# Kernel tuning notes

Hardware: AMD Instinct MI355X
Metric: run time of the kernel (lower is better)

The kernel has to match this reference:

```python
import jax, jax.numpy as jnp
import numpy as np
import math

B, H, W = 4, 128, 128
D_MODEL, D_HEAD, N_HEADS = 256, 64, 4
COND, D_FF = 256, 512
WS, SHIFT = 8, 4
EPS = 1e-6


def _make_masks(n_h, n_w, wh, ww, shift):
    # Swin-style shifted-window attention mask, vectorized (matches make_shifted_window_masks)
    ph = np.arange(n_h)[:, None, None, None, None, None]
    pw = np.arange(n_w)[None, :, None, None, None, None]
    qh = np.arange(wh)[None, None, :, None, None, None]
    qw = np.arange(ww)[None, None, None, :, None, None]
    kh = np.arange(wh)[None, None, None, None, :, None]
    kw = np.arange(ww)[None, None, None, None, None, :]
    is_top, is_left = ph == 0, pw == 0
    qa, ka, ql, kl = qh < shift, kh < shift, qw < shift, kw < shift
    m = ((is_left & is_top & (ql == kl) & (qa == ka))
         | (is_left & ~is_top & (ql == kl))
         | (~is_left & is_top & (qa == ka))
         | (~is_left & ~is_top))
    m = np.broadcast_to(m, (n_h, n_w, wh, ww, wh, ww))
    return jnp.asarray(m.reshape(n_h, n_w, wh * ww, wh * ww))


def _rms_norm(x, scale):
    ms = jnp.mean(jnp.square(x), -1, keepdims=True)
    return x * (scale * jax.lax.rsqrt(ms + EPS))


def _rope(x, theta):
    # rotate first 2*d dims of x (d = theta.shape[-1]), pass rest through
    d = theta.shape[-1]
    x1, x2, rest = x[..., :d], x[..., d:2 * d], x[..., 2 * d:]
    c, s = jnp.cos(theta), jnp.sin(theta)
    return jnp.concatenate([x1 * c - x2 * s, x2 * c + x1 * s, rest], axis=-1)


def setup_inputs() -> dict:
    key = jax.random.key(0)
    ks = jax.random.split(key, 10)
    x = jax.random.normal(ks[0], (B, H, W, D_MODEL), jnp.float32)
    gh = jnp.linspace(-1.0, 1.0, H)
    gw = jnp.linspace(-1.0, 1.0, W)
    pos = jnp.stack(jnp.meshgrid(gh, gw, indexing='ij'), axis=-1)  # [H,W,2]
    pos = jnp.broadcast_to(pos, (B, H, W, 2)).astype(jnp.float32)
    cond = jax.random.normal(ks[1], (B, COND), jnp.float32)
    # AdaRMSNorm linears are zero-init in torch; use small random so scale ~ 1
    norm1_w = 0.02 * jax.random.normal(ks[2], (D_MODEL, COND), jnp.float32)
    norm2_w = 0.02 * jax.random.normal(ks[3], (D_MODEL, COND), jnp.float32)
    qkv_w = jax.random.normal(ks[4], (3 * D_MODEL, D_MODEL), jnp.float32) / math.sqrt(D_MODEL)
    out_w = jax.random.normal(ks[5], (D_MODEL, D_MODEL), jnp.float32) / math.sqrt(D_MODEL)
    up_w = jax.random.normal(ks[6], (2 * D_FF, D_MODEL), jnp.float32) / math.sqrt(D_MODEL)
    down_w = jax.random.normal(ks[7], (D_MODEL, D_FF), jnp.float32) / math.sqrt(D_FF)
    scale_attn = jnp.full((N_HEADS,), 10.0, jnp.float32)
    # AxialRoPE freqs buffer: dim = d_head // 2
    dim = D_HEAD // 2
    f = np.exp(np.linspace(math.log(math.pi), math.log(10.0 * math.pi), N_HEADS * dim // 4 + 1)[:-1])
    freqs = jnp.asarray(f.reshape(dim // 4, N_HEADS).T, dtype=jnp.float32)  # [n_heads, d_head//8]
    return {"x": x, "pos": pos, "cond": cond, "norm1_w": norm1_w, "qkv_w": qkv_w,
            "scale_attn": scale_attn, "freqs": freqs, "out_w": out_w,
            "norm2_w": norm2_w, "up_w": up_w, "down_w": down_w}


def reference(x, pos, cond, norm1_w, qkv_w, scale_attn, freqs, out_w, norm2_w, up_w, down_w):
    b, h, w, dm = x.shape
    # --- shifted-window self-attention block ---
    skip = x
    xn = _rms_norm(x, (cond @ norm1_w.T + 1.0)[:, None, None, :])
    qkv = (xn @ qkv_w.T).reshape(b, h, w, 3, N_HEADS, D_HEAD)
    qkv = jnp.transpose(qkv, (3, 0, 4, 1, 2, 5))  # [3, b, nh, h, w, dh]
    q, k, v = qkv[0], qkv[1], qkv[2]
    # cosine-sim QK scaling with learned per-head scale
    s = jnp.sqrt(scale_attn)[None, :, None, None, None]
    q = q * (s * jax.lax.rsqrt(jnp.sum(q * q, -1, keepdims=True) + EPS))
    k = k * (s * jax.lax.rsqrt(jnp.sum(k * k, -1, keepdims=True) + EPS))
    # axial RoPE
    theta_h = pos[..., None, 0:1] * freqs  # [b,h,w,nh,dh//8]
    theta_w = pos[..., None, 1:2] * freqs
    theta = jnp.moveaxis(jnp.concatenate([theta_h, theta_w], -1), -2, -4)  # [b,nh,h,w,dh//4]
    q = _rope(q, theta)
    k = _rope(k, theta)
    # shifted windowing: roll, then partition into WS x WS windows
    def win(t):
        t = jnp.roll(t, (SHIFT, SHIFT), axis=(-3, -2))
        t = t.reshape(b, N_HEADS, h // WS, WS, w // WS, WS, D_HEAD)
        t = jnp.swapaxes(t, -4, -3)  # [b,nh,h',w',WS,WS,dh]
        return t.reshape(b, N_HEADS, h // WS, w // WS, WS * WS, D_HEAD)
    qw_, kw_, vw_ = win(q), win(k), win(v)
    mask = _make_masks(h // WS, w // WS, WS, WS, SHIFT)  # [h',w',S,S]
    scores = jnp.einsum('bnhwqd,bnhwkd->bnhwqk', qw_, kw_)  # sdpa scale=1.0 (cosine sim)
    scores = jnp.where(mask, scores, -1e30)
    attn = jax.nn.softmax(scores, axis=-1)
    o = jnp.einsum('bnhwqk,bnhwkd->bnhwqd', attn, vw_)
    # un-window and roll back
    o = o.reshape(b, N_HEADS, h // WS, w // WS, WS, WS, D_HEAD)
    o = jnp.swapaxes(o, -4, -3).reshape(b, N_HEADS, h, w, D_HEAD)
    o = jnp.roll(o, (-SHIFT, -SHIFT), axis=(-3, -2))
    o = jnp.transpose(o, (0, 2, 3, 1, 4)).reshape(b, h, w, dm)
    x = skip + o @ out_w.T
    # --- GEGLU feed-forward block ---
    skip = x
    xn = _rms_norm(x, (cond @ norm2_w.T + 1.0)[:, None, None, :])
    u = xn @ up_w.T
    a, g = u[..., :D_FF], u[..., D_FF:]
    x = skip + (a * jax.nn.gelu(g, approximate=False)) @ down_w.T
    return x
```

## Files before the change

kernel.cpp:

```cpp
#include <hip/hip_runtime.h>
#include <hip/hip_bf16.h>


using short8 = __attribute__((ext_vector_type(8))) short;
using f32x4  = __attribute__((ext_vector_type(4))) float;

#define DEVINL __device__ __forceinline__

DEVINL float bf2f(unsigned short u) {
    union { unsigned u; float f; } v; v.u = ((unsigned)u) << 16; return v.f;
}
DEVINL unsigned short f2bf(float f) {
    union { float f; unsigned u; } v; v.f = f;
    unsigned u = v.u;
    return (unsigned short)((u + 0x7FFFu + ((u >> 16) & 1u)) >> 16);
}
DEVINL void unpack8(uint4 pk, float* f) {
    unsigned w[4] = { pk.x, pk.y, pk.z, pk.w };
#pragma unroll
    for (int t = 0; t < 4; ++t) {
        union { unsigned u; float f; } lo, hi;
        lo.u = w[t] << 16; hi.u = w[t] & 0xffff0000u;
        f[2 * t] = lo.f; f[2 * t + 1] = hi.f;
    }
}
DEVINL void gload_lds16(const void* g, void* l) {
    __builtin_amdgcn_global_load_lds(
        (__attribute__((address_space(1))) void*)(unsigned long long)(uintptr_t)g,
        (__attribute__((address_space(3))) void*)(unsigned)(uintptr_t)l,
        16, 0, 0);
}

__global__ __launch_bounds__(256)
void wconv_kernel(const float* __restrict__ qkvw, const float* __restrict__ outw,
                  const float* __restrict__ upw, const float* __restrict__ downw,
                  unsigned short* __restrict__ dst)
{
    const int i = blockIdx.x * 256 + threadIdx.x;
    float v;
    if (i < 196608)      v = qkvw[i];
    else if (i < 262144) v = outw[i - 196608];
    else if (i < 524288) v = upw[i - 262144];
    else                 v = downw[i - 524288];
    dst[i] = f2bf(v);
}

__global__ __launch_bounds__(256)
void scales_kernel(const float* __restrict__ cond, const float* __restrict__ n1w,
                   const float* __restrict__ n2w, float* __restrict__ s1, float* __restrict__ s2)
{
    const int b = blockIdx.x & 3, which = blockIdx.x >> 2;
    const int c = threadIdx.x;
    const float* wrow = (which ? n2w : n1w) + (size_t)c * 256;
    const float* cb = cond + (size_t)b * 256;
    float acc = 0.f;
    for (int j = 0; j < 256; ++j) acc += cb[j] * wrow[j];
    (which ? s2 : s1)[b * 256 + c] = acc + 1.0f;
}

__global__ __launch_bounds__(256)
void rmsnorm_kernel(const float* __restrict__ x, const float* __restrict__ s,
                    unsigned short* __restrict__ out)
{
    const int t = blockIdx.x * 4 + (threadIdx.x >> 6);
    const int lane = threadIdx.x & 63;
    const float4 xv = *(const float4*)(x + (size_t)t * 256 + lane * 4);
    float ss = xv.x * xv.x + xv.y * xv.y + xv.z * xv.z + xv.w * xv.w;
#pragma unroll
    for (int off = 32; off; off >>= 1) ss += __shfl_xor(ss, off);
    const float rstd = rsqrtf(ss * (1.f / 256.f) + 1e-6f);
    const int b = t >> 14;
    const float4 sv = *(const float4*)(s + b * 256 + lane * 4);
    unsigned short o[4] = { f2bf(xv.x * sv.x * rstd), f2bf(xv.y * sv.y * rstd),
                            f2bf(xv.z * sv.z * rstd), f2bf(xv.w * sv.w * rstd) };
    *(uint2*)(out + (size_t)t * 256 + lane * 4) = *(uint2*)o;
}

template<int EPI>
__global__ __launch_bounds__(256)
void gemm_bt(const unsigned short* __restrict__ A, const unsigned short* __restrict__ Bw,
             const float* __restrict__ resid, void* __restrict__ outp,
             int M, int N, int K)
{
    __shared__ char smem[(EPI == 2) ? 49152 : 32768];
    const int tid = threadIdx.x;
    const int wave = tid >> 6, lane = tid & 63;
    const int n0 = blockIdx.x * 128;
    const int m0 = blockIdx.y * 128;
    const int wm = wave >> 1, wn = wave & 1;

    f32x4 acc[4][4] = {};
    f32x4 accg[4][4] = {};

    const int lrow8 = lane >> 3;
    const int skel = (lane & 7) * 8;

    for (int k0 = 0; k0 < K; k0 += 64) {
        __syncthreads();
#pragma unroll
        for (int i = 0; i < 4; ++i) {
            const int chunk = wave * 4 + i;
            const int row = chunk * 8 + lrow8;
            const unsigned short* ga = A  + (size_t)(m0 + row) * K + k0 + skel;
            const unsigned short* gb = Bw + (size_t)(n0 + row) * K + k0 + skel;
            gload_lds16(ga, smem + chunk * 1024);
            gload_lds16(gb, smem + 16384 + chunk * 1024);
            if constexpr (EPI == 2) {
                const unsigned short* gg = Bw + (size_t)(512 + n0 + row) * K + k0 + skel;
                gload_lds16(gg, smem + 32768 + chunk * 1024);
            }
        }
        __syncthreads();
#pragma unroll
        for (int kk = 0; kk < 2; ++kk) {
            const int kb = kk * 64 + (lane >> 4) * 16;
            short8 a[4], b[4], bg[4];
#pragma unroll
            for (int m = 0; m < 4; ++m)
                a[m] = *(const short8*)(smem + (wm * 64 + m * 16 + (lane & 15)) * 128 + kb);
#pragma unroll
            for (int n = 0; n < 4; ++n) {
                b[n] = *(const short8*)(smem + 16384 + (wn * 64 + n * 16 + (lane & 15)) * 128 + kb);
                if constexpr (EPI == 2)
                    bg[n] = *(const short8*)(smem + 32768 + (wn * 64 + n * 16 + (lane & 15)) * 128 + kb);
            }
#pragma unroll
            for (int m = 0; m < 4; ++m)
#pragma unroll
                for (int n = 0; n < 4; ++n) {
                    acc[m][n] = __builtin_amdgcn_mfma_f32_16x16x32_bf16(a[m], b[n], acc[m][n], 0, 0, 0);
                    if constexpr (EPI == 2)
                        accg[m][n] = __builtin_amdgcn_mfma_f32_16x16x32_bf16(a[m], bg[n], accg[m][n], 0, 0, 0);
                }
        }
    }
    const int rb = m0 + wm * 64 + ((lane >> 4) << 2);
    const int cb = n0 + wn * 64 + (lane & 15);
#pragma unroll
    for (int m = 0; m < 4; ++m)
#pragma unroll
        for (int n = 0; n < 4; ++n)
#pragma unroll
            for (int j = 0; j < 4; ++j) {
                const int row = rb + m * 16 + j;
                const int col = cb + n * 16;
                const size_t idx = (size_t)row * N + col;
                if constexpr (EPI == 0)
                    ((unsigned short*)outp)[idx] = f2bf(acc[m][n][j]);
                if constexpr (EPI == 1)
                    ((float*)outp)[idx] = resid[idx] + acc[m][n][j];
                if constexpr (EPI == 2) {
                    const float g = accg[m][n][j];
                    const float h = acc[m][n][j] * (0.5f * g * (1.0f + erff(g * 0.70710678118654752f)));
                    ((unsigned short*)outp)[idx] = f2bf(h);
                }
            }
}

__global__ __launch_bounds__(256)
void windowrope_kernel(const unsigned short* __restrict__ qkv, const float* __restrict__ pos,
                       const float* __restrict__ freqs, const float* __restrict__ sattn,
                       unsigned short* __restrict__ qw, unsigned short* __restrict__ kw,
                       unsigned short* __restrict__ vw)
{
    const int gid = blockIdx.x * 4 + (threadIdx.x >> 6);
    const int lane = threadIdx.x & 63;
    const int t = gid >> 2, n = gid & 3;
    const int b = t >> 14;
    const int h = (t >> 7) & 127, w = t & 127;

    const size_t base = (size_t)t * 768 + n * 64 + lane;
    float q = bf2f(qkv[base]);
    float k = bf2f(qkv[base + 256]);
    const float v = bf2f(qkv[base + 512]);

    float sq = q * q, sk = k * k;
#pragma unroll
    for (int off = 32; off; off >>= 1) { sq += __shfl_xor(sq, off); sk += __shfl_xor(sk, off); }
    const float sc = sqrtf(sattn[n]);
    q *= sc * rsqrtf(sq + 1e-6f);
    k *= sc * rsqrtf(sk + 1e-6f);

    const float qo = __shfl_xor(q, 16);
    const float ko = __shfl_xor(k, 16);
    if (lane < 32) {
        const int i = lane & 15;
        const float p = pos[(size_t)t * 2 + (i >> 3)];
        const float th = p * freqs[n * 8 + (i & 7)];
        float sth, cth;
        sincosf(th, &sth, &cth);
        if (lane < 16) { q = q * cth - qo * sth; k = k * cth - ko * sth; }
        else           { q = q * cth + qo * sth; k = k * cth + ko * sth; }
    }

    const int hr = (h + 4) & 127, wr = (w + 4) & 127;
    const int wh = hr >> 3, ww = wr >> 3;
    const int qp = (hr & 7) * 8 + (wr & 7);
    const size_t wbase = ((size_t)((b * 4 + n) * 256 + wh * 16 + ww) * 64 + qp) * 64 + lane;
    qw[wbase] = f2bf(q);
    kw[wbase] = f2bf(k);
    vw[wbase] = f2bf(v);
}

__global__ __launch_bounds__(64, 1)
void attn_kernel(const unsigned short* __restrict__ qw, const unsigned short* __restrict__ kw,
                 const unsigned short* __restrict__ vw, unsigned short* __restrict__ otok)
{
    __shared__ unsigned short Ks[4096];
    __shared__ unsigned short Vs[4096];
    const int bid = blockIdx.x;
    const int lane = threadIdx.x;
    const size_t wbase = (size_t)bid * 4096;

#pragma unroll
    for (int i = 0; i < 8; ++i) {
        const int idx = (i * 64 + lane) * 8;
        *(uint4*)(Ks + idx) = *(const uint4*)(kw + wbase + idx);
        *(uint4*)(Vs + idx) = *(const uint4*)(vw + wbase + idx);
    }
    float q[64];
#pragma unroll
    for (int i = 0; i < 8; ++i) {
        const uint4 pk = *(const uint4*)(qw + wbase + (size_t)lane * 64 + i * 8);
        unpack8(pk, q + i * 8);
    }
    __syncthreads();

    const int wh = (bid >> 4) & 15, ww = bid & 15;
    unsigned long long mask = ~0ull;
    if (wh == 0) mask &= (lane < 32) ? 0x00000000FFFFFFFFull : 0xFFFFFFFF00000000ull;
    if (ww == 0) mask &= ((lane & 7) < 4) ? 0x0F0F0F0F0F0F0F0Full : 0xF0F0F0F0F0F0F0F0ull;

    float o[64];
#pragma unroll
    for (int d = 0; d < 64; ++d) o[d] = 0.f;
    float sum = 0.f;

    for (int j = 0; j < 64; ++j) {
        float part[8];
#pragma unroll
        for (int dv = 0; dv < 8; ++dv) {
            const uint4 pk = *(const uint4*)(Ks + j * 64 + dv * 8);
            float f[8]; unpack8(pk, f);
            float a = 0.f;
#pragma unroll
            for (int u = 0; u < 8; ++u) a = fmaf(q[dv * 8 + u], f[u], a);
            part[dv] = a;
        }
        float s = ((part[0] + part[1]) + (part[2] + part[3])) +
                  ((part[4] + part[5]) + (part[6] + part[7]));
        float p = ((mask >> j) & 1ull) ? __expf(s - 10.f) : 0.f;
        sum += p;
#pragma unroll
        for (int dv = 0; dv < 8; ++dv) {
            const uint4 pk = *(const uint4*)(Vs + j * 64 + dv * 8);
            float f[8]; unpack8(pk, f);
#pragma unroll
            for (int u = 0; u < 8; ++u) o[dv * 8 + u] = fmaf(p, f[u], o[dv * 8 + u]);
        }
    }
    const float inv = 1.f / sum;

    const int b = bid >> 10, n = (bid >> 8) & 3;
    const int h = (wh * 8 + (lane >> 3) - 4) & 127;
    const int w = (ww * 8 + (lane & 7) - 4) & 127;
    unsigned short* dst = otok + ((size_t)(b * 128 + h) * 128 + w) * 256 + n * 64;
#pragma unroll
    for (int i = 0; i < 8; ++i) {
        unsigned short tmp[8];
#pragma unroll
        for (int u = 0; u < 8; ++u) tmp[u] = f2bf(o[i * 8 + u] * inv);
        *(uint4*)(dst + i * 8) = *(uint4*)tmp;
    }
}

extern "C" void kernel_launch(void* const* d_in, const int* in_sizes, int n_in,
                              void* d_out, int out_size, void* d_ws, size_t ws_size,
                              hipStream_t stream)
{
    (void)in_sizes; (void)n_in; (void)out_size; (void)ws_size;
    const float* x     = (const float*)d_in[0];
    const float* pos   = (const float*)d_in[1];
    const float* cond  = (const float*)d_in[2];
    const float* n1w   = (const float*)d_in[3];
    const float* qkvw  = (const float*)d_in[4];
    const float* sattn = (const float*)d_in[5];
    const float* freqs = (const float*)d_in[6];
    const float* outw  = (const float*)d_in[7];
    const float* n2w   = (const float*)d_in[8];
    const float* upw   = (const float*)d_in[9];
    const float* downw = (const float*)d_in[10];

    char* ws = (char*)d_ws;
    unsigned short* WB    = (unsigned short*)(ws);
    unsigned short* Wqkv  = WB;
    unsigned short* Wout  = WB + 196608;
    unsigned short* Wup   = WB + 262144;
    unsigned short* Wdown = WB + 524288;
    float* S1 = (float*)(ws + 1310720);
    float* S2 = (float*)(ws + 1314816);
    unsigned short* XN   = (unsigned short*)(ws + 2097152);
    unsigned short* QW   = (unsigned short*)(ws + 2097152);
    unsigned short* KW   = (unsigned short*)(ws + 35651584);
    unsigned short* VW   = (unsigned short*)(ws + 69206016);
    unsigned short* QKV  = (unsigned short*)(ws + 102760448);
    unsigned short* OTOK = (unsigned short*)(ws + 102760448);
    float*          X1   = (float*)(ws + 136314880);
    unsigned short* XN2  = (unsigned short*)(ws + 2097152);
    unsigned short* HG   = (unsigned short*)(ws + 35651584);

    wconv_kernel<<<2560, 256, 0, stream>>>(qkvw, outw, upw, downw, WB);
    scales_kernel<<<8, 256, 0, stream>>>(cond, n1w, n2w, S1, S2);
    rmsnorm_kernel<<<16384, 256, 0, stream>>>(x, S1, XN);
    gemm_bt<0><<<dim3(6, 512), 256, 0, stream>>>(XN, Wqkv, nullptr, QKV, 65536, 768, 256);
    windowrope_kernel<<<65536, 256, 0, stream>>>(QKV, pos, freqs, sattn, QW, KW, VW);
    attn_kernel<<<4096, 64, 0, stream>>>(QW, KW, VW, OTOK);
    gemm_bt<1><<<dim3(2, 512), 256, 0, stream>>>(OTOK, Wout, x, X1, 65536, 256, 256);
    rmsnorm_kernel<<<16384, 256, 0, stream>>>(X1, S2, XN2);
    gemm_bt<2><<<dim3(4, 512), 256, 0, stream>>>(XN2, Wup, nullptr, HG, 65536, 512, 256);
    gemm_bt<1><<<dim3(2, 512), 256, 0, stream>>>(HG, Wdown, X1, (float*)d_out, 65536, 256, 512);
}
```

Measured before the change: 623.2 us.

## Shrink GEMM N-tile to 64, add XOR-swizzled LDS, split up/gate GEMM

Halves the GEMM block tile in N from 128 to 64 and adds launch_bounds occupancy hints, which cuts accumulator registers and LDS per block so more blocks fit per CU. LDS rows are stored with an XOR swizzle, applied both on the global-to-LDS load and on the fragment reads, to avoid bank conflicts. The GEGLU up/gate GEMM moves into its own kernel with a 64-wide tile. The cost is twice as many blocks, each re-reading the A tile, so A-matrix global traffic doubles in exchange for better occupancy.

```diff
diff --git a/kernel.cpp b/kernel.cpp
--- a/kernel.cpp
+++ b/kernel.cpp
@@ -30,6 +30,7 @@
         (__attribute__((address_space(3))) void*)(unsigned)(uintptr_t)l,
         16, 0, 0);
 }
+DEVINL int swz(int row, int kb) { return row * 128 + (kb ^ ((row & 7) << 4)); }
 
 __global__ __launch_bounds__(256)
 void wconv_kernel(const float* __restrict__ qkvw, const float* __restrict__ outw,
@@ -77,69 +78,57 @@
 }
 
 template<int EPI>
-__global__ __launch_bounds__(256)
+__global__ __launch_bounds__(256, 4)
 void gemm_bt(const unsigned short* __restrict__ A, const unsigned short* __restrict__ Bw,
              const float* __restrict__ resid, void* __restrict__ outp,
              int M, int N, int K)
 {
-    __shared__ char smem[(EPI == 2) ? 49152 : 32768];
+    __shared__ char smem[24576];
     const int tid = threadIdx.x;
     const int wave = tid >> 6, lane = tid & 63;
-    const int n0 = blockIdx.x * 128;
+    const int n0 = blockIdx.x * 64;
     const int m0 = blockIdx.y * 128;
     const int wm = wave >> 1, wn = wave & 1;
 
-    f32x4 acc[4][4] = {};
-    f32x4 accg[4][4] = {};
+    f32x4 acc[4][2] = {};
 
     const int lrow8 = lane >> 3;
-    const int skel = (lane & 7) * 8;
+    const int skel = ((lane & 7) ^ lrow8) * 8;
 
     for (int k0 = 0; k0 < K; k0 += 64) {
         __syncthreads();
 #pragma unroll
-        for (int i = 0; i < 4; ++i) {
-            const int chunk = wave * 4 + i;
-            const int row = chunk * 8 + lrow8;
-            const unsigned short* ga = A  + (size_t)(m0 + row) * K + k0 + skel;
-            const unsigned short* gb = Bw + (size_t)(n0 + row) * K + k0 + skel;
-            gload_lds16(ga, smem + chunk * 1024);
-            gload_lds16(gb, smem + 16384 + chunk * 1024);
-            if constexpr (EPI == 2) {
-                const unsigned short* gg = Bw + (size_t)(512 + n0 + row) * K + k0 + skel;
-                gload_lds16(gg, smem + 32768 + chunk * 1024);
-            }
+        for (int i = 0; i < 6; ++i) {
+            const int cc = wave * 6 + i;
+            const unsigned short* src;
+            if (cc < 16) src = A  + (size_t)(m0 + cc * 8 + lrow8) * K + k0 + skel;
+            else         src = Bw + (size_t)(n0 + (cc - 16) * 8 + lrow8) * K + k0 + skel;
+            gload_lds16(src, smem + cc * 1024);
         }
         __syncthreads();
 #pragma unroll
         for (int kk = 0; kk < 2; ++kk) {
             const int kb = kk * 64 + (lane >> 4) * 16;
-            short8 a[4], b[4], bg[4];
+            short8 a[4], b[2];
 #pragma unroll
             for (int m = 0; m < 4; ++m)
-                a[m] = *(const short8*)(smem + (wm * 64 + m * 16 + (lane & 15)) * 128 + kb);
-#pragma unroll
-            for (int n = 0; n < 4; ++n) {
-                b[n] = *(const short8*)(smem + 16384 + (wn * 64 + n * 16 + (lane & 15)) * 128 + kb);
-                if constexpr (EPI == 2)
-                    bg[n] = *(const short8*)(smem + 32768 + (wn * 64 + n * 16 + (lane & 15)) * 128 + kb);
-            }
+                a[m] = *(const short8*)(smem + swz(wm * 64 + m * 16 + (lane & 15), kb));
+#pragma unroll
+            for (int n = 0; n < 2; ++n)
+                b[n] = *(const short8*)(smem + 16384 + swz(wn * 32 + n * 16 + (lane & 15), kb));
 #pragma unroll
             for (int m = 0; m < 4; ++m)
 #pragma unroll
-                for (int n = 0; n < 4; ++n) {
+                for (int n = 0; n < 2; ++n)
                     acc[m][n] = __builtin_amdgcn_mfma_f32_16x16x32_bf16(a[m], b[n], acc[m][n], 0, 0, 0);
-                    if constexpr (EPI == 2)
-                        accg[m][n] = __builtin_amdgcn_mfma_f32_16x16x32_bf16(a[m], bg[n], accg[m][n], 0, 0, 0);
-                }
         }
     }
     const int rb = m0 + wm * 64 + ((lane >> 4) << 2);
-    const int cb = n0 + wn * 64 + (lane & 15);
+    const int cb = n0 + wn * 32 + (lane & 15);
 #pragma unroll
     for (int m = 0; m < 4; ++m)
 #pragma unroll
-        for (int n = 0; n < 4; ++n)
+        for (int n = 0; n < 2; ++n)
 #pragma unroll
             for (int j = 0; j < 4; ++j) {
                 const int row = rb + m * 16 + j;
@@ -147,13 +136,76 @@
                 const size_t idx = (size_t)row * N + col;
                 if constexpr (EPI == 0)
                     ((unsigned short*)outp)[idx] = f2bf(acc[m][n][j]);
-                if constexpr (EPI == 1)
+                else
                     ((float*)outp)[idx] = resid[idx] + acc[m][n][j];
-                if constexpr (EPI == 2) {
-                    const float g = accg[m][n][j];
-                    const float h = acc[m][n][j] * (0.5f * g * (1.0f + erff(g * 0.70710678118654752f)));
-                    ((unsigned short*)outp)[idx] = f2bf(h);
+            }
+}
+
+__global__ __launch_bounds__(256, 2)
+void gemm_upgate(const unsigned short* __restrict__ A, const unsigned short* __restrict__ Bw,
+                 unsigned short* __restrict__ outp)
+{
+    __shared__ char smem[32768];
+    const int K = 256;
+    const int tid = threadIdx.x;
+    const int wave = tid >> 6, lane = tid & 63;
+    const int n0 = blockIdx.x * 64;
+    const int m0 = blockIdx.y * 128;
+    const int wm = wave >> 1, wn = wave & 1;
+
+    f32x4 acc[4][2] = {};
+    f32x4 accg[4][2] = {};
+
+    const int lrow8 = lane >> 3;
+    const int skel = ((lane & 7) ^ lrow8) * 8;
+
+    for (int k0 = 0; k0 < K; k0 += 64) {
+        __syncthreads();
+#pragma unroll
+        for (int i = 0; i < 8; ++i) {
+            const int cc = wave * 8 + i;
+            const unsigned short* src;
+            if (cc < 16)      src = A  + (size_t)(m0 + cc * 8 + lrow8) * K + k0 + skel;
+            else if (cc < 24) src = Bw + (size_t)(n0 + (cc - 16) * 8 + lrow8) * K + k0 + skel;
+            else              src = Bw + (size_t)(512 + n0 + (cc - 24) * 8 + lrow8) * K + k0 + skel;
+            gload_lds16(src, smem + cc * 1024);
+        }
+        __syncthreads();
+#pragma unroll
+        for (int kk = 0; kk < 2; ++kk) {
+            const int kb = kk * 64 + (lane >> 4) * 16;
+            short8 a[4], b[2], bg[2];
+#pragma unroll
+            for (int m = 0; m < 4; ++m)
+                a[m] = *(const short8*)(smem + swz(wm * 64 + m * 16 + (lane & 15), kb));
+#pragma unroll
+            for (int n = 0; n < 2; ++n) {
+                const int r = wn * 32 + n * 16 + (lane & 15);
+                b[n]  = *(const short8*)(smem + 16384 + swz(r, kb));
+                bg[n] = *(const short8*)(smem + 24576 + swz(r, kb));
+            }
+#pragma unroll
+            for (int m = 0; m < 4; ++m)
+#pragma unroll
+                for (int n = 0; n < 2; ++n) {
+                    acc[m][n]  = __builtin_amdgcn_mfma_f32_16x16x32_bf16(a[m], b[n],  acc[m][n],  0, 0, 0);
+                    accg[m][n] = __builtin_amdgcn_mfma_f32_16x16x32_bf16(a[m], bg[n], accg[m][n], 0, 0, 0);
                 }
+        }
+    }
+    const int rb = m0 + wm * 64 + ((lane >> 4) << 2);
+    const int cb = n0 + wn * 32 + (lane & 15);
+#pragma unroll
+    for (int m = 0; m < 4; ++m)
+#pragma unroll
+        for (int n = 0; n < 2; ++n)
+#pragma unroll
+            for (int j = 0; j < 4; ++j) {
+                const int row = rb + m * 16 + j;
+                const int col = cb + n * 16;
+                const float g = accg[m][n][j];
+                const float h = acc[m][n][j] * (0.5f * g * (1.0f + erff(g * 0.70710678118654752f)));
+                outp[(size_t)row * 512 + col] = f2bf(h);
             }
 }
 
@@ -312,11 +364,11 @@
     wconv_kernel<<<2560, 256, 0, stream>>>(qkvw, outw, upw, downw, WB);
     scales_kernel<<<8, 256, 0, stream>>>(cond, n1w, n2w, S1, S2);
     rmsnorm_kernel<<<16384, 256, 0, stream>>>(x, S1, XN);
-    gemm_bt<0><<<dim3(6, 512), 256, 0, stream>>>(XN, Wqkv, nullptr, QKV, 65536, 768, 256);
+    gemm_bt<0><<<dim3(12, 512), 256, 0, stream>>>(XN, Wqkv, nullptr, QKV, 65536, 768, 256);
     windowrope_kernel<<<65536, 256, 0, stream>>>(QKV, pos, freqs, sattn, QW, KW, VW);
     attn_kernel<<<4096, 64, 0, stream>>>(QW, KW, VW, OTOK);
-    gemm_bt<1><<<dim3(2, 512), 256, 0, stream>>>(OTOK, Wout, x, X1, 65536, 256, 256);
+    gemm_bt<1><<<dim3(4, 512), 256, 0, stream>>>(OTOK, Wout, x, X1, 65536, 256, 256);
     rmsnorm_kernel<<<16384, 256, 0, stream>>>(X1, S2, XN2);
-    gemm_bt<2><<<dim3(4, 512), 256, 0, stream>>>(XN2, Wup, nullptr, HG, 65536, 512, 256);
-    gemm_bt<1><<<dim3(2, 512), 256, 0, stream>>>(HG, Wdown, X1, (float*)d_out, 65536, 256, 512);
-}
+    gemm_upgate<<<dim3(8, 512), 256, 0, stream>>>(XN2, Wup, HG);
+    gemm_bt<1><<<dim3(4, 512), 256, 0, stream>>>(HG, Wdown, X1, (float*)d_out, 65536, 256, 512);
+}
```

Result: faster. 564.9 us (-9.4%).
